# Optimization experiments

Measured on AMD Instinct MI355X. Metric: run time of the kernel, lower is better.

Reference implementation:

```python
import jax, jax.numpy as jnp
import numpy as np

N = 8192
IN_F = 256
OUT_F = 256


def setup_inputs() -> dict:
    key = jax.random.key(0)
    k_v, k_adj, k1, k2, k3, kb = jax.random.split(key, 6)
    stdv = 1.0 / np.sqrt(OUT_F)
    V = jax.random.normal(k_v, (N, IN_F), dtype=jnp.float32)
    adj = jax.random.randint(k_adj, (N, N), 0, 4, dtype=jnp.int32)
    w1 = jax.random.uniform(k1, (IN_F, OUT_F), jnp.float32, -stdv, stdv)
    w2 = jax.random.uniform(k2, (IN_F, OUT_F), jnp.float32, -stdv, stdv)
    w3 = jax.random.uniform(k3, (IN_F, OUT_F), jnp.float32, -stdv, stdv)
    bias = jax.random.uniform(kb, (OUT_F,), jnp.float32, -stdv, stdv)
    return {"V": V, "adj": adj, "w1": w1, "w2": w2, "w3": w3, "bias": bias}


def reference(V, adj, w1, w2, w3, bias):
    # typed relational GCN: for each edge type k in {1,2,3},
    # aggregate (adj==k) @ (V @ wk), then sum and add bias
    o1 = jnp.matmul((adj == 1).astype(jnp.float32), jnp.matmul(V, w1))
    o2 = jnp.matmul((adj == 2).astype(jnp.float32), jnp.matmul(V, w2))
    o3 = jnp.matmul((adj == 3).astype(jnp.float32), jnp.matmul(V, w3))
    return o1 + o2 + o3 + bias
```

## Files before the change

### kernel.cpp

```cpp
#include <hip/hip_runtime.h>

typedef __attribute__((ext_vector_type(4))) float f32x4;
typedef __attribute__((ext_vector_type(16))) float f32x16;
typedef __attribute__((ext_vector_type(4))) unsigned short u16x4;
typedef __attribute__((ext_vector_type(4))) int i32x4;
typedef __attribute__((ext_vector_type(8))) __bf16 bf16x8;

union FragAB {
  u16x4 u[2];
  i32x4 v;
  bf16x8 f;
};

static __device__ __forceinline__ unsigned short f2bf(float x) {
  union { float f; unsigned u; } v;
  v.f = x;
  unsigned r = v.u + 0x7FFFu + ((v.u >> 16) & 1u);
  return (unsigned short)(r >> 16);
}

#define NN 8192

__global__ __launch_bounds__(256) void k_prep(const int* __restrict__ adj,
                                              const float* __restrict__ bias,
                                              unsigned char* __restrict__ adj2b,
                                              float* __restrict__ out) {
  int t = blockIdx.x * 256 + threadIdx.x;
  int nT = gridDim.x * 256;
  for (int g = t; g < 16777216; g += nT) {
    i32x4 a = *(const i32x4*)(adj + (size_t)g * 4);
    adj2b[g] = (unsigned char)((a.x & 3) | ((a.y & 3) << 2) |
                               ((a.z & 3) << 4) | ((a.w & 3) << 6));
  }
  for (int g = t; g < 524288; g += nT) {
    *(f32x4*)(out + (size_t)g * 4) = *(const f32x4*)(bias + ((g * 4) & 255));
  }
}

__global__ __launch_bounds__(256) void k_transform(
    const float* __restrict__ V, const float* __restrict__ w1,
    const float* __restrict__ w2, const float* __restrict__ w3,
    unsigned short* __restrict__ Bp) {
  int bx = blockIdx.x;
  int rb = bx & 63;
  int nb = bx >> 6;
  const float* W = (nb < 4) ? w1 : (nb < 8) ? w2 : w3;
  int nc0 = (nb & 3) * 64;
  int tid = threadIdx.x;
  int lane = tid & 63;
  int wv = tid >> 6;
  int wm = wv >> 1, wn = wv & 1;
  int q = lane >> 4, l16 = lane & 15;

  __shared__ unsigned short tA[128][36];
  __shared__ unsigned short tB[64][36];

  f32x4 acc[4][2];
#pragma unroll
  for (int i = 0; i < 4; i++)
#pragma unroll
    for (int j = 0; j < 2; j++) acc[i][j] = (f32x4)0.0f;

  for (int kk = 0; kk < 256; kk += 32) {
    {
      int r = tid >> 1, c0 = (tid & 1) * 16;
      const float* src = V + (size_t)(rb * 128 + r) * 256 + kk + c0;
      f32x4 f0 = *(const f32x4*)(src + 0);
      f32x4 f1 = *(const f32x4*)(src + 4);
      f32x4 f2 = *(const f32x4*)(src + 8);
      f32x4 f3 = *(const f32x4*)(src + 12);
      unsigned short* d = &tA[r][c0];
      d[0] = f2bf(f0.x);  d[1] = f2bf(f0.y);  d[2] = f2bf(f0.z);  d[3] = f2bf(f0.w);
      d[4] = f2bf(f1.x);  d[5] = f2bf(f1.y);  d[6] = f2bf(f1.z);  d[7] = f2bf(f1.w);
      d[8] = f2bf(f2.x);  d[9] = f2bf(f2.y);  d[10] = f2bf(f2.z); d[11] = f2bf(f2.w);
      d[12] = f2bf(f3.x); d[13] = f2bf(f3.y); d[14] = f2bf(f3.z); d[15] = f2bf(f3.w);
    }
    {
      int r = tid >> 3, c0 = (tid & 7) * 8;
      const float* src = W + (size_t)(kk + r) * 256 + nc0 + c0;
      f32x4 g0 = *(const f32x4*)(src);
      f32x4 g1 = *(const f32x4*)(src + 4);
      tB[c0 + 0][r] = f2bf(g0.x); tB[c0 + 1][r] = f2bf(g0.y);
      tB[c0 + 2][r] = f2bf(g0.z); tB[c0 + 3][r] = f2bf(g0.w);
      tB[c0 + 4][r] = f2bf(g1.x); tB[c0 + 5][r] = f2bf(g1.y);
      tB[c0 + 6][r] = f2bf(g1.z); tB[c0 + 7][r] = f2bf(g1.w);
    }
    __syncthreads();
    FragAB af[4], bf[2];
#pragma unroll
    for (int mt = 0; mt < 4; mt++) {
      const unsigned short* p = &tA[wm * 64 + mt * 16 + l16][q * 8];
      af[mt].u[0] = *(const u16x4*)p;
      af[mt].u[1] = *(const u16x4*)(p + 4);
    }
#pragma unroll
    for (int nt = 0; nt < 2; nt++) {
      const unsigned short* p = &tB[wn * 32 + nt * 16 + l16][q * 8];
      bf[nt].u[0] = *(const u16x4*)p;
      bf[nt].u[1] = *(const u16x4*)(p + 4);
    }
#pragma unroll
    for (int mt = 0; mt < 4; mt++)
#pragma unroll
      for (int nt = 0; nt < 2; nt++)
        acc[mt][nt] = __builtin_amdgcn_mfma_f32_16x16x32_bf16(
            af[mt].f, bf[nt].f, acc[mt][nt], 0, 0, 0);
    __syncthreads();
  }
  int ty = nb >> 2;
#pragma unroll
  for (int mt = 0; mt < 4; mt++)
#pragma unroll
    for (int nt = 0; nt < 2; nt++) {
      int n = (nb & 3) * 64 + wn * 32 + nt * 16 + l16;
      int j0 = rb * 128 + wm * 64 + mt * 16 + q * 4;
      u16x4 hv;
      hv.x = f2bf(acc[mt][nt].x);
      hv.y = f2bf(acc[mt][nt].y);
      hv.z = f2bf(acc[mt][nt].z);
      hv.w = f2bf(acc[mt][nt].w);
      size_t idx = (size_t)ty * 2097152 + (size_t)(j0 >> 4) * 4096 + n * 16 + (j0 & 15);
      *(u16x4*)(Bp + idx) = hv;
    }
}

__global__ __launch_bounds__(256, 2) void k_agg(const unsigned* __restrict__ adj2,
                                                const unsigned short* __restrict__ Bp,
                                                float* __restrict__ out) {
  int bx = blockIdx.x;
  int ks = bx & 7, rb = bx >> 3;
  int tid = threadIdx.x, lane = tid & 63;
  int wv = tid >> 6;
  int wm = wv >> 1, wn = wv & 1;
  int q = lane >> 5, l32 = lane & 31;
  int qsh = q << 4;

  f32x16 acc[2][4];
#pragma unroll
  for (int mt = 0; mt < 2; mt++)
#pragma unroll
    for (int nt = 0; nt < 4; nt++) acc[mt][nt] = (f32x16)0.0f;

  int r0 = rb * 128 + wm * 64 + l32;
  const unsigned* ap0 = adj2 + (size_t)r0 * 512 + ks * 64;
  const unsigned* ap1 = ap0 + 32 * 512;

  int nbase = (wn * 128 + l32) * 16 + q * 8;
  const unsigned short* bb[3][2];
#pragma unroll
  for (int ty = 0; ty < 3; ty++)
#pragma unroll
    for (int kh = 0; kh < 2; kh++)
      bb[ty][kh] = Bp + (size_t)ty * 2097152 + ((size_t)ks * 64 + kh) * 4096 + nbase;

  unsigned long long c0 = *(const unsigned long long*)ap0;
  unsigned long long c1 = *(const unsigned long long*)ap1;

  for (int step = 0; step < 32; ++step) {
    unsigned long long nx0 = 0, nx1 = 0;
    if (step < 31) {
      nx0 = *(const unsigned long long*)(ap0 + 2 * (step + 1));
      nx1 = *(const unsigned long long*)(ap1 + 2 * (step + 1));
    }
    FragAB bv0[3][4];
#pragma unroll
    for (int ty = 0; ty < 3; ty++)
#pragma unroll
      for (int nt = 0; nt < 4; nt++)
        bv0[ty][nt].v = *(const i32x4*)(bb[ty][0] + nt * 512);
    {
      unsigned w0 = (unsigned)c0 >> qsh;
      unsigned w1 = (unsigned)c1 >> qsh;
#pragma unroll
      for (int ty = 0; ty < 3; ty++) {
        FragAB A0, A1;
#pragma unroll
        for (int d = 0; d < 4; d++) {
          unsigned p00 = (w0 >> (4 * d)) & 3u, p01 = (w0 >> (4 * d + 2)) & 3u;
          unsigned p10 = (w1 >> (4 * d)) & 3u, p11 = (w1 >> (4 * d + 2)) & 3u;
          A0.v[d] = (int)((p00 == (unsigned)(ty + 1) ? 0x3F80u : 0u) |
                          (p01 == (unsigned)(ty + 1) ? 0x3F800000u : 0u));
          A1.v[d] = (int)((p10 == (unsigned)(ty + 1) ? 0x3F80u : 0u) |
                          (p11 == (unsigned)(ty + 1) ? 0x3F800000u : 0u));
        }
#pragma unroll
        for (int nt = 0; nt < 4; nt++) {
          acc[0][nt] = __builtin_amdgcn_mfma_f32_32x32x16_bf16(
              A0.f, bv0[ty][nt].f, acc[0][nt], 0, 0, 0);
          acc[1][nt] = __builtin_amdgcn_mfma_f32_32x32x16_bf16(
              A1.f, bv0[ty][nt].f, acc[1][nt], 0, 0, 0);
        }
      }
    }
    FragAB bv1[3][4];
#pragma unroll
    for (int ty = 0; ty < 3; ty++)
#pragma unroll
      for (int nt = 0; nt < 4; nt++)
        bv1[ty][nt].v = *(const i32x4*)(bb[ty][1] + nt * 512);
    {
      unsigned w0 = (unsigned)(c0 >> 32) >> qsh;
      unsigned w1 = (unsigned)(c1 >> 32) >> qsh;
#pragma unroll
      for (int ty = 0; ty < 3; ty++) {
        FragAB A0, A1;
#pragma unroll
        for (int d = 0; d < 4; d++) {
          unsigned p00 = (w0 >> (4 * d)) & 3u, p01 = (w0 >> (4 * d + 2)) & 3u;
          unsigned p10 = (w1 >> (4 * d)) & 3u, p11 = (w1 >> (4 * d + 2)) & 3u;
          A0.v[d] = (int)((p00 == (unsigned)(ty + 1) ? 0x3F80u : 0u) |
                          (p01 == (unsigned)(ty + 1) ? 0x3F800000u : 0u));
          A1.v[d] = (int)((p10 == (unsigned)(ty + 1) ? 0x3F80u : 0u) |
                          (p11 == (unsigned)(ty + 1) ? 0x3F800000u : 0u));
        }
#pragma unroll
        for (int nt = 0; nt < 4; nt++) {
          acc[0][nt] = __builtin_amdgcn_mfma_f32_32x32x16_bf16(
              A0.f, bv1[ty][nt].f, acc[0][nt], 0, 0, 0);
          acc[1][nt] = __builtin_amdgcn_mfma_f32_32x32x16_bf16(
              A1.f, bv1[ty][nt].f, acc[1][nt], 0, 0, 0);
        }
      }
    }
#pragma unroll
    for (int ty = 0; ty < 3; ty++)
#pragma unroll
      for (int kh = 0; kh < 2; kh++) bb[ty][kh] += 8192;
    c0 = nx0;
    c1 = nx1;
  }
#pragma unroll
  for (int mt = 0; mt < 2; mt++)
#pragma unroll
    for (int nt = 0; nt < 4; nt++) {
      int col = wn * 128 + nt * 32 + l32;
      int rowb = rb * 128 + wm * 64 + mt * 32 + 4 * q;
#pragma unroll
      for (int r = 0; r < 16; r++) {
        int row = rowb + (r & 3) + 8 * (r >> 2);
        atomicAdd(out + (size_t)row * 256 + col, acc[mt][nt][r]);
      }
    }
}

extern "C" void kernel_launch(void* const* d_in, const int* in_sizes, int n_in,
                              void* d_out, int out_size, void* d_ws,
                              size_t ws_size, hipStream_t stream) {
  const float* V = (const float*)d_in[0];
  const int* adj = (const int*)d_in[1];
  const float* w1 = (const float*)d_in[2];
  const float* w2 = (const float*)d_in[3];
  const float* w3 = (const float*)d_in[4];
  const float* bias = (const float*)d_in[5];
  float* out = (float*)d_out;
  unsigned short* Bp = (unsigned short*)d_ws;
  unsigned char* adj2b = (unsigned char*)d_ws + 0xC00000;

  k_prep<<<dim3(2048), dim3(256), 0, stream>>>(adj, bias, adj2b, out);
  k_transform<<<dim3(768), dim3(256), 0, stream>>>(V, w1, w2, w3, Bp);
  k_agg<<<dim3(512), dim3(256), 0, stream>>>((const unsigned*)adj2b, Bp, out);
}
```

Before: 499.8 us.

## Pre-convert V and weights to bf16 fragment layout in prep kernel

The prep kernel now converts V and the three weight matrices to bf16 and stores them in a k-blocked layout that matches the MFMA fragment loads. The transform kernel then reads fragments straight from global memory, with no shared-memory staging, no in-loop conversions and no barriers, and it uses a new tile shape (64 rows by 128 columns spanning weight types). This removes the redundant per-block fp32 to bf16 conversion and the LDS round trip. In exchange it adds an extra global write and read of the bf16 copies, and the weight scatter writes in prep are uncoalesced.

```diff
diff --git a/kernel.cpp b/kernel.cpp
--- a/kernel.cpp
+++ b/kernel.cpp
@@ -21,10 +21,12 @@
 
 #define NN 8192
 
-__global__ __launch_bounds__(256) void k_prep(const int* __restrict__ adj,
-                                              const float* __restrict__ bias,
-                                              unsigned char* __restrict__ adj2b,
-                                              float* __restrict__ out) {
+__global__ __launch_bounds__(256) void k_prep(
+    const int* __restrict__ adj, const float* __restrict__ V,
+    const float* __restrict__ w1, const float* __restrict__ w2,
+    const float* __restrict__ w3, const float* __restrict__ bias,
+    unsigned char* __restrict__ adj2b, unsigned short* __restrict__ Vbp,
+    unsigned short* __restrict__ Wbp, float* __restrict__ out) {
   int t = blockIdx.x * 256 + threadIdx.x;
   int nT = gridDim.x * 256;
   for (int g = t; g < 16777216; g += nT) {
@@ -33,93 +35,80 @@
                                ((a.z & 3) << 4) | ((a.w & 3) << 6));
   }
   for (int g = t; g < 524288; g += nT) {
+    int f = g * 4;
+    int row = f >> 8, kcol = f & 255;
+    f32x4 x = *(const f32x4*)(V + (size_t)f);
+    u16x4 h;
+    h.x = f2bf(x.x); h.y = f2bf(x.y); h.z = f2bf(x.z); h.w = f2bf(x.w);
+    *(u16x4*)(Vbp + (size_t)(kcol >> 3) * 65536 + (size_t)row * 8 + (kcol & 7)) = h;
+  }
+  for (int e = t; e < 65536; e += nT) {
+    int k = e >> 8, n = e & 255;
+    Wbp[(size_t)(k >> 3) * 6144 + (size_t)(0 * 256 + n) * 8 + (k & 7)] = f2bf(w1[e]);
+  }
+  for (int e = t; e < 65536; e += nT) {
+    int k = e >> 8, n = e & 255;
+    Wbp[(size_t)(k >> 3) * 6144 + (size_t)(1 * 256 + n) * 8 + (k & 7)] = f2bf(w2[e]);
+  }
+  for (int e = t; e < 65536; e += nT) {
+    int k = e >> 8, n = e & 255;
+    Wbp[(size_t)(k >> 3) * 6144 + (size_t)(2 * 256 + n) * 8 + (k & 7)] = f2bf(w3[e]);
+  }
+  for (int g = t; g < 524288; g += nT) {
     *(f32x4*)(out + (size_t)g * 4) = *(const f32x4*)(bias + ((g * 4) & 255));
   }
 }
 
 __global__ __launch_bounds__(256) void k_transform(
-    const float* __restrict__ V, const float* __restrict__ w1,
-    const float* __restrict__ w2, const float* __restrict__ w3,
+    const unsigned short* __restrict__ Vbp, const unsigned short* __restrict__ Wbp,
     unsigned short* __restrict__ Bp) {
   int bx = blockIdx.x;
-  int rb = bx & 63;
-  int nb = bx >> 6;
-  const float* W = (nb < 4) ? w1 : (nb < 8) ? w2 : w3;
-  int nc0 = (nb & 3) * 64;
-  int tid = threadIdx.x;
-  int lane = tid & 63;
+  int rb = bx & 127, nb = bx >> 7;
+  int tid = threadIdx.x, lane = tid & 63;
   int wv = tid >> 6;
-  int wm = wv >> 1, wn = wv & 1;
+  int wr = wv >> 1, wc = wv & 1;
   int q = lane >> 4, l16 = lane & 15;
 
-  __shared__ unsigned short tA[128][36];
-  __shared__ unsigned short tB[64][36];
-
-  f32x4 acc[4][2];
-#pragma unroll
-  for (int i = 0; i < 4; i++)
-#pragma unroll
-    for (int j = 0; j < 2; j++) acc[i][j] = (f32x4)0.0f;
-
+  f32x4 acc[2][4];
+#pragma unroll
+  for (int i = 0; i < 2; i++)
+#pragma unroll
+    for (int j = 0; j < 4; j++) acc[i][j] = (f32x4)0.0f;
+
+  int r0 = rb * 64 + wr * 32 + l16;
+  int n0 = nb * 128 + wc * 64 + l16;
+  const unsigned short* av = Vbp + (size_t)q * 65536 + (size_t)r0 * 8;
+  const unsigned short* bv = Wbp + (size_t)q * 6144 + (size_t)n0 * 8;
+
+#pragma unroll 2
   for (int kk = 0; kk < 256; kk += 32) {
-    {
-      int r = tid >> 1, c0 = (tid & 1) * 16;
-      const float* src = V + (size_t)(rb * 128 + r) * 256 + kk + c0;
-      f32x4 f0 = *(const f32x4*)(src + 0);
-      f32x4 f1 = *(const f32x4*)(src + 4);
-      f32x4 f2 = *(const f32x4*)(src + 8);
-      f32x4 f3 = *(const f32x4*)(src + 12);
-      unsigned short* d = &tA[r][c0];
-      d[0] = f2bf(f0.x);  d[1] = f2bf(f0.y);  d[2] = f2bf(f0.z);  d[3] = f2bf(f0.w);
-      d[4] = f2bf(f1.x);  d[5] = f2bf(f1.y);  d[6] = f2bf(f1.z);  d[7] = f2bf(f1.w);
-      d[8] = f2bf(f2.x);  d[9] = f2bf(f2.y);  d[10] = f2bf(f2.z); d[11] = f2bf(f2.w);
-      d[12] = f2bf(f3.x); d[13] = f2bf(f3.y); d[14] = f2bf(f3.z); d[15] = f2bf(f3.w);
-    }
-    {
-      int r = tid >> 3, c0 = (tid & 7) * 8;
-      const float* src = W + (size_t)(kk + r) * 256 + nc0 + c0;
-      f32x4 g0 = *(const f32x4*)(src);
-      f32x4 g1 = *(const f32x4*)(src + 4);
-      tB[c0 + 0][r] = f2bf(g0.x); tB[c0 + 1][r] = f2bf(g0.y);
-      tB[c0 + 2][r] = f2bf(g0.z); tB[c0 + 3][r] = f2bf(g0.w);
-      tB[c0 + 4][r] = f2bf(g1.x); tB[c0 + 5][r] = f2bf(g1.y);
-      tB[c0 + 6][r] = f2bf(g1.z); tB[c0 + 7][r] = f2bf(g1.w);
-    }
-    __syncthreads();
-    FragAB af[4], bf[2];
-#pragma unroll
-    for (int mt = 0; mt < 4; mt++) {
-      const unsigned short* p = &tA[wm * 64 + mt * 16 + l16][q * 8];
-      af[mt].u[0] = *(const u16x4*)p;
-      af[mt].u[1] = *(const u16x4*)(p + 4);
-    }
-#pragma unroll
-    for (int nt = 0; nt < 2; nt++) {
-      const unsigned short* p = &tB[wn * 32 + nt * 16 + l16][q * 8];
-      bf[nt].u[0] = *(const u16x4*)p;
-      bf[nt].u[1] = *(const u16x4*)(p + 4);
-    }
-#pragma unroll
-    for (int mt = 0; mt < 4; mt++)
-#pragma unroll
-      for (int nt = 0; nt < 2; nt++)
+    FragAB af[2], bf[4];
+#pragma unroll
+    for (int mt = 0; mt < 2; mt++)
+      af[mt].v = *(const i32x4*)(av + (size_t)(kk >> 3) * 65536 + mt * 128);
+#pragma unroll
+    for (int nt = 0; nt < 4; nt++)
+      bf[nt].v = *(const i32x4*)(bv + (size_t)(kk >> 3) * 6144 + nt * 128);
+#pragma unroll
+    for (int mt = 0; mt < 2; mt++)
+#pragma unroll
+      for (int nt = 0; nt < 4; nt++)
         acc[mt][nt] = __builtin_amdgcn_mfma_f32_16x16x32_bf16(
             af[mt].f, bf[nt].f, acc[mt][nt], 0, 0, 0);
-    __syncthreads();
-  }
-  int ty = nb >> 2;
-#pragma unroll
-  for (int mt = 0; mt < 4; mt++)
-#pragma unroll
-    for (int nt = 0; nt < 2; nt++) {
-      int n = (nb & 3) * 64 + wn * 32 + nt * 16 + l16;
-      int j0 = rb * 128 + wm * 64 + mt * 16 + q * 4;
+  }
+#pragma unroll
+  for (int mt = 0; mt < 2; mt++)
+#pragma unroll
+    for (int nt = 0; nt < 4; nt++) {
+      int n = n0 + nt * 16;
+      int ty = n >> 8, nn = n & 255;
+      int j0 = rb * 64 + wr * 32 + mt * 16 + q * 4;
       u16x4 hv;
       hv.x = f2bf(acc[mt][nt].x);
       hv.y = f2bf(acc[mt][nt].y);
       hv.z = f2bf(acc[mt][nt].z);
       hv.w = f2bf(acc[mt][nt].w);
-      size_t idx = (size_t)ty * 2097152 + (size_t)(j0 >> 4) * 4096 + n * 16 + (j0 & 15);
+      size_t idx = (size_t)ty * 2097152 + (size_t)(j0 >> 4) * 4096 + nn * 16 + (j0 & 15);
       *(u16x4*)(Bp + idx) = hv;
     }
 }
@@ -255,8 +244,11 @@
   float* out = (float*)d_out;
   unsigned short* Bp = (unsigned short*)d_ws;
   unsigned char* adj2b = (unsigned char*)d_ws + 0xC00000;
-
-  k_prep<<<dim3(2048), dim3(256), 0, stream>>>(adj, bias, adj2b, out);
-  k_transform<<<dim3(768), dim3(256), 0, stream>>>(V, w1, w2, w3, Bp);
+  unsigned short* Vbp = (unsigned short*)((char*)d_ws + 0x1C00000);
+  unsigned short* Wbp = (unsigned short*)((char*)d_ws + 0x2000000);
+
+  k_prep<<<dim3(2048), dim3(256), 0, stream>>>(adj, V, w1, w2, w3, bias, adj2b,
+                                               Vbp, Wbp, out);
+  k_transform<<<dim3(768), dim3(256), 0, stream>>>(Vbp, Wbp, Bp);
   k_agg<<<dim3(512), dim3(256), 0, stream>>>((const unsigned*)adj2b, Bp, out);
 }
```

Result: no change. 499.7 us (-0.0%).
